# Kernel tuning notes

Measured on AMD Instinct MI355X. Metric: run time of the kernel, lower is better.

## Reference

```python
import jax, jax.numpy as jnp
import numpy as np

NUM_HEADS = 32
HEAD_DIM = 128
HIDDEN = NUM_HEADS * HEAD_DIM
BLOCK = 128
ROPE_THETA = 10000.0
NEG_INF = -1e9


def _fp4_e2m1(x):
    # Simulated float_quantize(x, exp=2, man=1): E2M1 grid {0, .5, 1, 1.5, 2, 3, 4, 6},
    # round-to-nearest-even, saturate at +-6.
    a = jnp.abs(x)
    e = jnp.clip(jnp.floor(jnp.log2(jnp.maximum(a, 1e-30))), 0.0, 2.0)
    step = jnp.exp2(e) * 0.5  # mantissa LSB at this exponent
    q = jnp.clip(jnp.round(a / step) * step, 0.0, 6.0)
    return jnp.sign(x) * q


def quantize_mxfp4(v, block=BLOCK):
    # along_rows=False path: block over the sequence axis (after transpose(-1,-2)).
    b, h, s, d = v.shape
    t = jnp.swapaxes(v, -1, -2)  # [b,h,d,s]
    pad = (-s) % block
    t = jnp.pad(t, ((0, 0), (0, 0), (0, 0), (0, pad)))
    t = t.reshape(-1, block)
    amax = jnp.max(jnp.abs(t), axis=-1, keepdims=True)
    scale = jnp.exp2(jnp.ceil(jnp.log2(jnp.maximum(amax, 1e-30))) - 3.0)
    scale = jnp.where(amax == 0, 1.0, scale)
    t = _fp4_e2m1(t / scale) * scale
    t = t.reshape(b, h, d, s + pad)[..., :s]
    return jnp.swapaxes(t, -1, -2)


def _rotary(position_ids, dtype):
    # cos/sin: [b, s, head_dim]
    inv_freq = 1.0 / (ROPE_THETA ** (jnp.arange(0, HEAD_DIM, 2, dtype=jnp.float32) / HEAD_DIM))
    freqs = position_ids.astype(jnp.float32)[..., None] * inv_freq  # [b,s,d/2]
    emb = jnp.concatenate([freqs, freqs], axis=-1)
    return jnp.cos(emb).astype(dtype), jnp.sin(emb).astype(dtype)


def _rotate_half(x):
    x1, x2 = jnp.split(x, 2, axis=-1)
    return jnp.concatenate([-x2, x1], axis=-1)


def setup_inputs() -> dict:
    key = jax.random.key(0)
    ks = jax.random.split(key, 5)
    wscale = 1.0 / np.sqrt(HIDDEN)
    return {
        "hidden_states": jax.random.normal(ks[0], (2, 2048, HIDDEN), dtype=jnp.float32),
        "position_ids": jnp.arange(2048, dtype=jnp.int32)[None, :],
        "Wq": jax.random.normal(ks[1], (HIDDEN, HIDDEN), dtype=jnp.float32) * wscale,
        "Wk": jax.random.normal(ks[2], (HIDDEN, HIDDEN), dtype=jnp.float32) * wscale,
        "Wv": jax.random.normal(ks[3], (HIDDEN, HIDDEN), dtype=jnp.float32) * wscale,
        "Wo": jax.random.normal(ks[4], (HIDDEN, HIDDEN), dtype=jnp.float32) * wscale,
    }


def reference(hidden_states, position_ids, Wq, Wk, Wv, Wo):
    b, s, _ = hidden_states.shape

    # per-head channel ordering from ||row of v_proj||_2 (descending)
    norm3 = jnp.linalg.norm(Wv.astype(jnp.float32), ord=2, axis=-1)  # [HIDDEN]
    order = jnp.argsort(-norm3.reshape(NUM_HEADS, HEAD_DIM), axis=-1)  # [H, D]
    inverse_order = jnp.argsort(order, axis=-1)

    def proj(W):
        y = jnp.einsum('bsh,oh->bso', hidden_states, W)
        return y.reshape(b, s, NUM_HEADS, HEAD_DIM).transpose(0, 2, 1, 3)  # [b,H,s,D]

    q = proj(Wq)
    k = proj(Wk)
    v = proj(Wv)

    # reorder channels, mxfp4-quantize V along sequence blocks, restore order
    v = jnp.take_along_axis(v, order[None, :, None, :], axis=-1)
    v = quantize_mxfp4(v, BLOCK)
    v = jnp.take_along_axis(v, inverse_order[None, :, None, :], axis=-1)

    cos, sin = _rotary(position_ids, hidden_states.dtype)
    cos = cos[:, None, :, :]  # unsqueeze_dim=1
    sin = sin[:, None, :, :]
    q = q * cos + _rotate_half(q) * sin
    k = k * cos + _rotate_half(k) * sin

    scores = jnp.einsum('bhqd,bhkd->bhqk', q, k) / np.sqrt(HEAD_DIM)
    causal = jnp.tril(jnp.ones((s, s), dtype=bool))
    scores = jnp.where(causal[None, None], scores, NEG_INF)
    attn = jax.nn.softmax(scores.astype(jnp.float32), axis=-1).astype(q.dtype)

    out = jnp.einsum('bhqk,bhkd->bhqd', attn, v)
    out = out.transpose(0, 2, 1, 3).reshape(b, s, HIDDEN)
    return jnp.einsum('bso,ho->bsh', out, Wo)
```

## Files before the change

### kernel.cpp

```cpp
#include <hip/hip_runtime.h>
#include <math.h>

typedef unsigned short u16;
typedef unsigned int u32;
typedef short bf16x8 __attribute__((ext_vector_type(8)));
typedef float f32x4 __attribute__((ext_vector_type(4)));

#define MFMA16(a, b, c) __builtin_amdgcn_mfma_f32_16x16x32_bf16(a, b, c, 0, 0, 0)

static __device__ __forceinline__ u16 f2b(float f) {
  u32 u = __builtin_bit_cast(u32, f);
  u = (u + 0x7fffu + ((u >> 16) & 1u)) >> 16;
  return (u16)u;
}
static __device__ __forceinline__ float b2f(u16 h) {
  return __builtin_bit_cast(float, ((u32)h) << 16);
}
static __device__ __forceinline__ void gload16(const void* g, void* l) {
  __builtin_amdgcn_global_load_lds((const __attribute__((address_space(1))) void*)g,
                                   (__attribute__((address_space(3))) void*)l, 16, 0, 0);
}
static __device__ __forceinline__ void split2(float x, u16& hi, u16& lo) {
  hi = f2b(x);
  lo = f2b(x - b2f(hi));
}
static __device__ __forceinline__ float quant1(float x, float scale, float rs) {
  float y = fabsf(x) * rs;
  float st = y < 2.f ? 0.5f : (y < 4.f ? 1.f : 2.f);
  float iv = y < 2.f ? 2.f : (y < 4.f ? 1.f : 0.5f);
  float q = fminf(rintf(y * iv) * st, 6.f);
  return copysignf(q * scale, x);
}

__global__ __launch_bounds__(256) void k_cvt(const float* __restrict__ in, u16* __restrict__ out) {
  int i = blockIdx.x * 256 + threadIdx.x;
  float4 v = ((const float4*)in)[i];
  u32 lo = (u32)f2b(v.x) | ((u32)f2b(v.y) << 16);
  u32 hi = (u32)f2b(v.z) | ((u32)f2b(v.w) << 16);
  ((uint2*)out)[i] = make_uint2(lo, hi);
}

__global__ __launch_bounds__(256) void k_splt(const float* __restrict__ in,
                                              u16* __restrict__ hi, u16* __restrict__ lo) {
  int i = blockIdx.x * 256 + threadIdx.x;
  float4 v = ((const float4*)in)[i];
  u16 h[4], l[4];
  split2(v.x, h[0], l[0]);
  split2(v.y, h[1], l[1]);
  split2(v.z, h[2], l[2]);
  split2(v.w, h[3], l[3]);
  ((uint2*)hi)[i] = make_uint2((u32)h[0] | ((u32)h[1] << 16), (u32)h[2] | ((u32)h[3] << 16));
  ((uint2*)lo)[i] = make_uint2((u32)l[0] | ((u32)l[1] << 16), (u32)l[2] | ((u32)l[3] << 16));
}

__global__ __launch_bounds__(256) void k_rope_tab(const int* __restrict__ pid,
                                                  float* __restrict__ ct,
                                                  float* __restrict__ st) {
  int t = blockIdx.x * 256 + threadIdx.x;
  int s = t >> 6, i = t & 63;
  float inv = powf(10000.f, -(float)i * (1.f / 64.f));
  float a = (float)pid[s] * inv;
  ct[t] = cosf(a);
  st[t] = sinf(a);
}

template <int EPI>
__global__ __launch_bounds__(512, 2) void k_gemm8(const u16* __restrict__ A,
                                                  const u16* __restrict__ B,
                                                  void* __restrict__ outp,
                                                  const float* __restrict__ cost,
                                                  const float* __restrict__ sint) {
  __shared__ u16 Ls[2][2][2][8192];
  const int tid = threadIdx.x;
  const int wid = tid >> 6, lane = tid & 63;
  const int l15 = lane & 15, lhi = lane >> 4;
  const int wm = wid >> 2, wn = wid & 3;
  const int hib = wn >> 1, sub = wn & 1;

  const int bid = blockIdx.x;
  const int bx = 2 * (bid & 7) + (bid >> 7);
  const int by = (bid >> 3) & 15;
  const int mbase = by * 256, nbase = bx * 256;

  f32x4 acc[8][4];
#pragma unroll
  for (int mi = 0; mi < 8; ++mi)
#pragma unroll
    for (int nj = 0; nj < 4; ++nj) acc[mi][nj] = (f32x4){0.f, 0.f, 0.f, 0.f};

  auto stA = [&](int buf, int half, int ktile) {
    u16* dst = Ls[buf][0][half];
    const int k0 = ktile * 64;
#pragma unroll
    for (int i = 0; i < 2; ++i) {
      int idx = i * 512 + tid;
      int row = idx >> 3;
      int col = k0 + ((((idx & 7) << 4) ^ ((row & 7) << 4)) >> 1);
      gload16(A + (size_t)(mbase + half * 128 + row) * 4096 + col, (char*)dst + idx * 16);
    }
  };
  auto stB = [&](int buf, int half, int ktile) {
    u16* dst = Ls[buf][1][half];
    const int k0 = ktile * 64;
#pragma unroll
    for (int i = 0; i < 2; ++i) {
      int idx = i * 512 + tid;
      int row = idx >> 3;
      int col = k0 + ((((idx & 7) << 4) ^ ((row & 7) << 4)) >> 1);
      gload16(B + (size_t)(nbase + half * 128 + row) * 4096 + col, (char*)dst + idx * 16);
    }
  };

  stB(0, 0, 0);
  stB(0, 1, 0);
  stA(0, 0, 0);
  stA(0, 1, 0);
  stB(1, 0, 1);
  stB(1, 1, 1);

  const int NT = 64;
  for (int kt = 0; kt < NT; ++kt) {
    const int cur = kt & 1, nxt = cur ^ 1;
    const u16* Ab = Ls[cur][0][wm];
    const u16* Bb = Ls[cur][1][hib];
    bf16x8 aA[4][2], aB[4][2], bA[2][2], bB[2][2];

    if (kt + 1 < NT) stA(nxt, 0, kt + 1);
    if (kt == NT - 1) {
      asm volatile("s_waitcnt vmcnt(0)" ::: "memory");
    } else {
      asm volatile("s_waitcnt vmcnt(6)" ::: "memory");
    }
    __builtin_amdgcn_s_barrier();
#pragma unroll
    for (int mi = 0; mi < 4; ++mi)
#pragma unroll
      for (int ks = 0; ks < 2; ++ks) {
        int row = mi * 16 + l15;
        int kk2 = (ks * 32 + lhi * 8) * 2;
        aA[mi][ks] = *(const bf16x8*)((const char*)Ab + row * 128 + (kk2 ^ ((row & 7) << 4)));
      }
#pragma unroll
    for (int nj = 0; nj < 2; ++nj)
#pragma unroll
      for (int ks = 0; ks < 2; ++ks) {
        int row = sub * 32 + nj * 16 + l15;
        int kk2 = (ks * 32 + lhi * 8) * 2;
        bA[nj][ks] = *(const bf16x8*)((const char*)Bb + row * 128 + (kk2 ^ ((row & 7) << 4)));
      }
    __builtin_amdgcn_s_setprio(1);
#pragma unroll
    for (int mi = 0; mi < 4; ++mi)
#pragma unroll
      for (int nj = 0; nj < 2; ++nj)
#pragma unroll
        for (int ks = 0; ks < 2; ++ks) acc[mi][nj] = MFMA16(aA[mi][ks], bA[nj][ks], acc[mi][nj]);
    __builtin_amdgcn_s_setprio(0);
    __builtin_amdgcn_s_barrier();

#pragma unroll
    for (int nj = 0; nj < 2; ++nj)
#pragma unroll
      for (int ks = 0; ks < 2; ++ks) {
        int row = 64 + sub * 32 + nj * 16 + l15;
        int kk2 = (ks * 32 + lhi * 8) * 2;
        bB[nj][ks] = *(const bf16x8*)((const char*)Bb + row * 128 + (kk2 ^ ((row & 7) << 4)));
      }
    if (kt + 1 < NT) stA(nxt, 1, kt + 1);
    __builtin_amdgcn_s_barrier();
    __builtin_amdgcn_s_setprio(1);
#pragma unroll
    for (int mi = 0; mi < 4; ++mi)
#pragma unroll
      for (int nj = 0; nj < 2; ++nj)
#pragma unroll
        for (int ks = 0; ks < 2; ++ks)
          acc[mi][nj + 2] = MFMA16(aA[mi][ks], bB[nj][ks], acc[mi][nj + 2]);
    __builtin_amdgcn_s_setprio(0);
    __builtin_amdgcn_s_barrier();

#pragma unroll
    for (int mi = 0; mi < 4; ++mi)
#pragma unroll
      for (int ks = 0; ks < 2; ++ks) {
        int row = 64 + mi * 16 + l15;
        int kk2 = (ks * 32 + lhi * 8) * 2;
        aB[mi][ks] = *(const bf16x8*)((const char*)Ab + row * 128 + (kk2 ^ ((row & 7) << 4)));
      }
    if (kt + 2 < NT) stB(cur, 0, kt + 2);
    __builtin_amdgcn_s_barrier();
    __builtin_amdgcn_s_setprio(1);
#pragma unroll
    for (int mi = 0; mi < 4; ++mi)
#pragma unroll
      for (int nj = 0; nj < 2; ++nj)
#pragma unroll
        for (int ks = 0; ks < 2; ++ks)
          acc[mi + 4][nj] = MFMA16(aB[mi][ks], bA[nj][ks], acc[mi + 4][nj]);
    __builtin_amdgcn_s_setprio(0);
    __builtin_amdgcn_s_barrier();

    if (kt + 2 < NT) stB(cur, 1, kt + 2);
    __builtin_amdgcn_s_barrier();
    __builtin_amdgcn_s_setprio(1);
#pragma unroll
    for (int mi = 0; mi < 4; ++mi)
#pragma unroll
      for (int nj = 0; nj < 2; ++nj)
#pragma unroll
        for (int ks = 0; ks < 2; ++ks)
          acc[mi + 4][nj + 2] = MFMA16(aB[mi][ks], bB[nj][ks], acc[mi + 4][nj + 2]);
    __builtin_amdgcn_s_setprio(0);
    __builtin_amdgcn_s_barrier();
  }

  if constexpr (EPI == 3) {
    float* out = (float*)outp;
#pragma unroll
    for (int mi = 0; mi < 8; ++mi)
#pragma unroll
      for (int r = 0; r < 4; ++r) {
        size_t m = (size_t)(mbase + wm * 128 + mi * 16 + lhi * 4 + r);
#pragma unroll
        for (int nj = 0; nj < 4; ++nj) {
          int n = nbase + hib * 128 + (nj >> 1) * 64 + sub * 32 + (nj & 1) * 16 + l15;
          out[m * 4096 + n] = acc[mi][nj][r];
        }
      }
  } else {
    u16* qo = (u16*)outp;
    const int hgl = bx * 2 + hib;
#pragma unroll
    for (int mi = 0; mi < 8; ++mi)
#pragma unroll
      for (int r = 0; r < 4; ++r) {
        int m = mbase + wm * 128 + mi * 16 + lhi * 4 + r;
        int b = m >> 11, s = m & 2047;
        const float* ct = cost + (size_t)s * 64;
        const float* st = sint + (size_t)s * 64;
        size_t base = ((size_t)(b * 32 + hgl) * 2048 + s) * 128;
#pragma unroll
        for (int nj = 0; nj < 2; ++nj) {
          int d = sub * 32 + nj * 16 + l15;
          float c = ct[d], sn = st[d];
          float x1 = acc[mi][nj][r], x2 = acc[mi][nj + 2][r];
          qo[base + d] = f2b(x1 * c - x2 * sn);
          qo[base + d + 64] = f2b(x2 * c + x1 * sn);
        }
      }
  }
}

__global__ __launch_bounds__(256) void k_gemmv2(const u16* __restrict__ ahi,
                                                const u16* __restrict__ alo,
                                                const u16* __restrict__ bhi,
                                                const u16* __restrict__ blo,
                                                u16* __restrict__ vt) {
  __shared__ u16 AsHi[128 * 64];
  __shared__ u16 AsLo[128 * 64];
  __shared__ u16 BsHi[128 * 64];
  __shared__ u16 BsLo[128 * 64];
  const int tid = threadIdx.x;
  const int w = tid >> 6, lane = tid & 63;
  const int l15 = lane & 15, lhi = lane >> 4;
  const int mbase = blockIdx.y * 128, nbase = blockIdx.x * 128;
  f32x4 acc[2][8];
#pragma unroll
  for (int i = 0; i < 2; ++i)
#pragma unroll
    for (int j = 0; j < 8; ++j) acc[i][j] = (f32x4){0.f, 0.f, 0.f, 0.f};

  for (int kt = 0; kt < 64; ++kt) {
    const int k0 = kt * 64;
#pragma unroll
    for (int i = 0; i < 4; ++i) {
      int idx = i * 256 + tid;
      int row = idx >> 3;
      int col = (k0 + ((((idx & 7) << 4) ^ ((row & 7) << 4)) >> 1));
      size_t ga = (size_t)(mbase + row) * 4096 + col;
      size_t gb = (size_t)(nbase + row) * 4096 + col;
      gload16(ahi + ga, (char*)AsHi + idx * 16);
      gload16(alo + ga, (char*)AsLo + idx * 16);
      gload16(bhi + gb, (char*)BsHi + idx * 16);
      gload16(blo + gb, (char*)BsLo + idx * 16);
    }
    __syncthreads();
#pragma unroll
    for (int ks = 0; ks < 2; ++ks) {
      const int kk2 = (ks * 32 + lhi * 8) * 2;
      bf16x8 afh[2], afl[2];
#pragma unroll
      for (int i = 0; i < 2; ++i) {
        int row = w * 32 + i * 16 + l15;
        int off = row * 128 + (kk2 ^ ((row & 7) << 4));
        afh[i] = *(const bf16x8*)((const char*)AsHi + off);
        afl[i] = *(const bf16x8*)((const char*)AsLo + off);
      }
#pragma unroll
      for (int j = 0; j < 8; ++j) {
        int row = j * 16 + l15;
        int off = row * 128 + (kk2 ^ ((row & 7) << 4));
        bf16x8 bh = *(const bf16x8*)((const char*)BsHi + off);
        bf16x8 bl = *(const bf16x8*)((const char*)BsLo + off);
#pragma unroll
        for (int i = 0; i < 2; ++i) {
          acc[i][j] = MFMA16(afh[i], bh, acc[i][j]);
          acc[i][j] = MFMA16(afh[i], bl, acc[i][j]);
          acc[i][j] = MFMA16(afl[i], bh, acc[i][j]);
        }
      }
    }
    __syncthreads();
  }

  const int h = nbase >> 7;
  float pam[8];
#pragma unroll
  for (int j = 0; j < 8; ++j) {
    float a = 0.f;
#pragma unroll
    for (int i = 0; i < 2; ++i)
#pragma unroll
      for (int r = 0; r < 4; ++r) a = fmaxf(a, fabsf(acc[i][j][r]));
    a = fmaxf(a, __shfl_xor(a, 16));
    a = fmaxf(a, __shfl_xor(a, 32));
    pam[j] = a;
  }
  float* red = (float*)BsHi;
  if (lhi == 0) {
#pragma unroll
    for (int j = 0; j < 8; ++j) red[w * 128 + j * 16 + l15] = pam[j];
  }
  __syncthreads();
#pragma unroll
  for (int j = 0; j < 8; ++j) {
    float amax = fmaxf(fmaxf(red[0 * 128 + j * 16 + l15], red[1 * 128 + j * 16 + l15]),
                       fmaxf(red[2 * 128 + j * 16 + l15], red[3 * 128 + j * 16 + l15]));
    float scale = 1.f, rs = 1.f;
    if (amax > 0.f) {
      int e;
      float mant = frexpf(amax, &e);
      int c = (mant == 0.5f) ? (e - 1) : e;
      scale = ldexpf(1.f, c - 3);
      rs = ldexpf(1.f, 3 - c);
    }
#pragma unroll
    for (int i = 0; i < 2; ++i) {
      int m0 = mbase + w * 32 + i * 16 + lhi * 4;
      int b = m0 >> 11, s0 = m0 & 2047;
      int d = j * 16 + l15;
      uint2 pk;
      float v0 = quant1(acc[i][j][0], scale, rs);
      float v1 = quant1(acc[i][j][1], scale, rs);
      float v2 = quant1(acc[i][j][2], scale, rs);
      float v3 = quant1(acc[i][j][3], scale, rs);
      pk.x = (u32)f2b(v0) | ((u32)f2b(v1) << 16);
      pk.y = (u32)f2b(v2) | ((u32)f2b(v3) << 16);
      *(uint2*)(vt + ((size_t)(b * 32 + h) * 128 + d) * 2048 + s0) = pk;
    }
  }
}

template <int EPI>
__global__ __launch_bounds__(256) void k_gemm(const u16* __restrict__ A,
                                              const float* __restrict__ B,
                                              void* __restrict__ outp,
                                              const float* __restrict__ cost,
                                              const float* __restrict__ sint) {
  __shared__ u16 As[128 * 64];
  __shared__ u16 Bs[128 * 64];
  const int tid = threadIdx.x;
  const int w = tid >> 6, lane = tid & 63;
  const int l15 = lane & 15, lhi = lane >> 4;
  const int mbase = blockIdx.y * 128, nbase = blockIdx.x * 128;
  f32x4 acc[2][8];
#pragma unroll
  for (int i = 0; i < 2; ++i)
#pragma unroll
    for (int j = 0; j < 8; ++j) acc[i][j] = (f32x4){0.f, 0.f, 0.f, 0.f};

  const int brow = tid >> 1, bk = (tid & 1) * 32;
  const float* bsrc = B + (size_t)(nbase + brow) * 4096 + bk;

  for (int kt = 0; kt < 64; ++kt) {
    const int k0 = kt * 64;
#pragma unroll
    for (int i = 0; i < 4; ++i) {
      int idx = i * 256 + tid;
      int row = idx >> 3;
      int inb = ((idx & 7) << 4) ^ ((row & 7) << 4);
      gload16(A + (size_t)(mbase + row) * 4096 + (k0 + (inb >> 1)), (char*)As + idx * 16);
    }
    float4 bv[8];
    const float* bp = bsrc + k0;
#pragma unroll
    for (int c = 0; c < 8; ++c) bv[c] = *(const float4*)(bp + c * 4);
#pragma unroll
    for (int c = 0; c < 4; ++c) {
      uint4 pk;
      pk.x = (u32)f2b(bv[2 * c].x) | ((u32)f2b(bv[2 * c].y) << 16);
      pk.y = (u32)f2b(bv[2 * c].z) | ((u32)f2b(bv[2 * c].w) << 16);
      pk.z = (u32)f2b(bv[2 * c + 1].x) | ((u32)f2b(bv[2 * c + 1].y) << 16);
      pk.w = (u32)f2b(bv[2 * c + 1].z) | ((u32)f2b(bv[2 * c + 1].w) << 16);
      int byte = brow * 128 + (((bk + c * 8) * 2) ^ ((brow & 7) << 4));
      *(uint4*)((char*)Bs + byte) = pk;
    }
    __syncthreads();
#pragma unroll
    for (int ks = 0; ks < 2; ++ks) {
      const int kk2 = (ks * 32 + lhi * 8) * 2;
      bf16x8 af[2], bfr[8];
#pragma unroll
      for (int i = 0; i < 2; ++i) {
        int row = w * 32 + i * 16 + l15;
        af[i] = *(const bf16x8*)((const char*)As + row * 128 + (kk2 ^ ((row & 7) << 4)));
      }
#pragma unroll
      for (int j = 0; j < 8; ++j) {
        int row = j * 16 + l15;
        bfr[j] = *(const bf16x8*)((const char*)Bs + row * 128 + (kk2 ^ ((row & 7) << 4)));
      }
#pragma unroll
      for (int i = 0; i < 2; ++i)
#pragma unroll
        for (int j = 0; j < 8; ++j) acc[i][j] = MFMA16(af[i], bfr[j], acc[i][j]);
    }
    __syncthreads();
  }

  const int h = nbase >> 7;
  if constexpr (EPI == 3) {
    float* out = (float*)outp;
#pragma unroll
    for (int i = 0; i < 2; ++i)
#pragma unroll
      for (int r = 0; r < 4; ++r) {
        size_t m = (size_t)(mbase + w * 32 + i * 16 + lhi * 4 + r);
#pragma unroll
        for (int j = 0; j < 8; ++j) out[m * 4096 + nbase + j * 16 + l15] = acc[i][j][r];
      }
  } else {
    u16* qo = (u16*)outp;
#pragma unroll
    for (int i = 0; i < 2; ++i)
#pragma unroll
      for (int r = 0; r < 4; ++r) {
        int m = mbase + w * 32 + i * 16 + lhi * 4 + r;
        int b = m >> 11, s = m & 2047;
        const float* ct = cost + (size_t)s * 64;
        const float* st = sint + (size_t)s * 64;
        size_t base = ((size_t)(b * 32 + h) * 2048 + s) * 128;
#pragma unroll
        for (int j = 0; j < 4; ++j) {
          int d = j * 16 + l15;
          float c = ct[d], sn = st[d];
          float x1 = acc[i][j][r], x2 = acc[i][j + 4][r];
          qo[base + d] = f2b(x1 * c - x2 * sn);
          qo[base + d + 64] = f2b(x2 * c + x1 * sn);
        }
      }
  }
}

__global__ __launch_bounds__(256) void k_gemmv(const float* __restrict__ hsf,
                                               const float* __restrict__ Wv,
                                               u16* __restrict__ vt) {
  __shared__ u16 AsHi[128 * 64];
  __shared__ u16 AsLo[128 * 64];
  __shared__ u16 BsHi[128 * 64];
  __shared__ u16 BsLo[128 * 64];
  const int tid = threadIdx.x;
  const int w = tid >> 6, lane = tid & 63;
  const int l15 = lane & 15, lhi = lane >> 4;
  const int mbase = blockIdx.y * 128, nbase = blockIdx.x * 128;
  f32x4 acc[2][8];
#pragma unroll
  for (int i = 0; i < 2; ++i)
#pragma unroll
    for (int j = 0; j < 8; ++j) acc[i][j] = (f32x4){0.f, 0.f, 0.f, 0.f};

  const int srow = tid >> 1, sk = (tid & 1) * 32;
  const float* asrc = hsf + (size_t)(mbase + srow) * 4096 + sk;
  const float* bsrc = Wv + (size_t)(nbase + srow) * 4096 + sk;

  for (int kt = 0; kt < 64; ++kt) {
    const int k0 = kt * 64;
    float4 av[8], bv[8];
#pragma unroll
    for (int c = 0; c < 8; ++c) {
      av[c] = *(const float4*)(asrc + k0 + c * 4);
      bv[c] = *(const float4*)(bsrc + k0 + c * 4);
    }
#pragma unroll
    for (int c = 0; c < 4; ++c) {
      u16 h0, l0, h1, l1;
      float fa[8] = {av[2 * c].x, av[2 * c].y, av[2 * c].z, av[2 * c].w,
                     av[2 * c + 1].x, av[2 * c + 1].y, av[2 * c + 1].z, av[2 * c + 1].w};
      float fb[8] = {bv[2 * c].x, bv[2 * c].y, bv[2 * c].z, bv[2 * c].w,
                     bv[2 * c + 1].x, bv[2 * c + 1].y, bv[2 * c + 1].z, bv[2 * c + 1].w};
      u32 ph[4], pl[4], qh[4], ql[4];
#pragma unroll
      for (int t = 0; t < 4; ++t) {
        split2(fa[2 * t], h0, l0);
        split2(fa[2 * t + 1], h1, l1);
        ph[t] = (u32)h0 | ((u32)h1 << 16);
        pl[t] = (u32)l0 | ((u32)l1 << 16);
        split2(fb[2 * t], h0, l0);
        split2(fb[2 * t + 1], h1, l1);
        qh[t] = (u32)h0 | ((u32)h1 << 16);
        ql[t] = (u32)l0 | ((u32)l1 << 16);
      }
      int byte = srow * 128 + (((sk + c * 8) * 2) ^ ((srow & 7) << 4));
      *(uint4*)((char*)AsHi + byte) = make_uint4(ph[0], ph[1], ph[2], ph[3]);
      *(uint4*)((char*)AsLo + byte) = make_uint4(pl[0], pl[1], pl[2], pl[3]);
      *(uint4*)((char*)BsHi + byte) = make_uint4(qh[0], qh[1], qh[2], qh[3]);
      *(uint4*)((char*)BsLo + byte) = make_uint4(ql[0], ql[1], ql[2], ql[3]);
    }
    __syncthreads();
#pragma unroll
    for (int ks = 0; ks < 2; ++ks) {
      const int kk2 = (ks * 32 + lhi * 8) * 2;
      bf16x8 afh[2], afl[2];
#pragma unroll
      for (int i = 0; i < 2; ++i) {
        int row = w * 32 + i * 16 + l15;
        int off = row * 128 + (kk2 ^ ((row & 7) << 4));
        afh[i] = *(const bf16x8*)((const char*)AsHi + off);
        afl[i] = *(const bf16x8*)((const char*)AsLo + off);
      }
#pragma unroll
      for (int j = 0; j < 8; ++j) {
        int row = j * 16 + l15;
        int off = row * 128 + (kk2 ^ ((row & 7) << 4));
        bf16x8 bh = *(const bf16x8*)((const char*)BsHi + off);
        bf16x8 bl = *(const bf16x8*)((const char*)BsLo + off);
#pragma unroll
        for (int i = 0; i < 2; ++i) {
          acc[i][j] = MFMA16(afh[i], bh, acc[i][j]);
          acc[i][j] = MFMA16(afh[i], bl, acc[i][j]);
          acc[i][j] = MFMA16(afl[i], bh, acc[i][j]);
        }
      }
    }
    __syncthreads();
  }

  const int h = nbase >> 7;
  float pam[8];
#pragma unroll
  for (int j = 0; j < 8; ++j) {
    float a = 0.f;
#pragma unroll
    for (int i = 0; i < 2; ++i)
#pragma unroll
      for (int r = 0; r < 4; ++r) a = fmaxf(a, fabsf(acc[i][j][r]));
    a = fmaxf(a, __shfl_xor(a, 16));
    a = fmaxf(a, __shfl_xor(a, 32));
    pam[j] = a;
  }
  float* red = (float*)BsHi;
  if (lhi == 0) {
#pragma unroll
    for (int j = 0; j < 8; ++j) red[w * 128 + j * 16 + l15] = pam[j];
  }
  __syncthreads();
#pragma unroll
  for (int j = 0; j < 8; ++j) {
    float amax = fmaxf(fmaxf(red[0 * 128 + j * 16 + l15], red[1 * 128 + j * 16 + l15]),
                       fmaxf(red[2 * 128 + j * 16 + l15], red[3 * 128 + j * 16 + l15]));
    float scale = 1.f, rs = 1.f;
    if (amax > 0.f) {
      int e;
      float mant = frexpf(amax, &e);
      int c = (mant == 0.5f) ? (e - 1) : e;
      scale = ldexpf(1.f, c - 3);
      rs = ldexpf(1.f, 3 - c);
    }
#pragma unroll
    for (int i = 0; i < 2; ++i) {
      int m0 = mbase + w * 32 + i * 16 + lhi * 4;
      int b = m0 >> 11, s0 = m0 & 2047;
      int d = j * 16 + l15;
      uint2 pk;
      float v0 = quant1(acc[i][j][0], scale, rs);
      float v1 = quant1(acc[i][j][1], scale, rs);
      float v2 = quant1(acc[i][j][2], scale, rs);
      float v3 = quant1(acc[i][j][3], scale, rs);
      pk.x = (u32)f2b(v0) | ((u32)f2b(v1) << 16);
      pk.y = (u32)f2b(v2) | ((u32)f2b(v3) << 16);
      *(uint2*)(vt + ((size_t)(b * 32 + h) * 128 + d) * 2048 + s0) = pk;
    }
  }
}

__global__ __launch_bounds__(512) void k_attn(const u16* __restrict__ qg,
                                              const u16* __restrict__ kg,
                                              const u16* __restrict__ vtg,
                                              u16* __restrict__ ao) {
  __shared__ u16 Ks[2][64 * 128];
  __shared__ u16 Vs[2][128 * 64];
  __shared__ u16 Ps[8 * 16 * 72];
  const int qt = 15 - blockIdx.y;
  const int bh = blockIdx.x;
  const int tid = threadIdx.x, w = tid >> 6, lane = tid & 63;
  const int l15 = lane & 15, lhi = lane >> 4;
  const size_t bhoff = (size_t)bh * (2048 * 128);
  const float SC = 0.08838834764831845f;

  bf16x8 qf[4];
  {
    const int qrow = qt * 128 + w * 16 + l15;
    const u16* qp = qg + bhoff + (size_t)qrow * 128 + lhi * 8;
#pragma unroll
    for (int ks = 0; ks < 4; ++ks) qf[ks] = *(const bf16x8*)(qp + ks * 32);
  }
  f32x4 oacc[8];
#pragma unroll
  for (int dt = 0; dt < 8; ++dt) oacc[dt] = (f32x4){0.f, 0.f, 0.f, 0.f};
  float mrow[4] = {-1e30f, -1e30f, -1e30f, -1e30f};
  float lrow[4] = {0.f, 0.f, 0.f, 0.f};

  auto stage = [&](int buf, int kbase) {
#pragma unroll
    for (int i = 0; i < 2; ++i) {
      int idx = i * 512 + tid;
      int row = idx >> 4;
      int inb = ((idx & 15) << 4) ^ ((row & 15) << 4);
      gload16(kg + bhoff + (size_t)(kbase + row) * 128 + (inb >> 1), (char*)Ks[buf] + idx * 16);
    }
#pragma unroll
    for (int i = 0; i < 2; ++i) {
      int idx = i * 512 + tid;
      int row = idx >> 3;
      int inb = ((idx & 7) << 4) ^ ((row & 7) << 4);
      gload16(vtg + bhoff + (size_t)row * 2048 + kbase + (inb >> 1), (char*)Vs[buf] + idx * 16);
    }
  };

  const int nt = 2 * qt + 2;
  stage(0, 0);

  for (int kt = 0; kt < nt; ++kt) {
    const int cur = kt & 1;
    if (kt < nt - 1) {
      stage(cur ^ 1, (kt + 1) * 64);
      asm volatile("s_waitcnt vmcnt(4)" ::: "memory");
    } else {
      asm volatile("s_waitcnt vmcnt(0)" ::: "memory");
    }
    __builtin_amdgcn_s_barrier();

    f32x4 sc4[4];
#pragma unroll
    for (int j = 0; j < 4; ++j) sc4[j] = (f32x4){0.f, 0.f, 0.f, 0.f};
#pragma unroll
    for (int ks = 0; ks < 4; ++ks) {
      const int db = (ks * 32 + lhi * 8) * 2;
#pragma unroll
      for (int j = 0; j < 4; ++j) {
        int kr = j * 16 + l15;
        bf16x8 bfr = *(const bf16x8*)((const char*)Ks[cur] + kr * 256 + (db ^ ((kr & 15) << 4)));
        sc4[j] = MFMA16(qf[ks], bfr, sc4[j]);
      }
    }
    float p[4][4];
    const int kbase = kt * 64;
    const bool tail = (kt >= 2 * qt);
#pragma unroll
    for (int j = 0; j < 4; ++j)
#pragma unroll
      for (int r = 0; r < 4; ++r) {
        float s = sc4[j][r] * SC;
        if (tail && (kbase + j * 16 + l15 > qt * 128 + w * 16 + lhi * 4 + r)) s = -1e9f;
        p[j][r] = s;
      }
    float alpha[4];
#pragma unroll
    for (int r = 0; r < 4; ++r) {
      float tm = fmaxf(fmaxf(p[0][r], p[1][r]), fmaxf(p[2][r], p[3][r]));
      tm = fmaxf(tm, __shfl_xor(tm, 1));
      tm = fmaxf(tm, __shfl_xor(tm, 2));
      tm = fmaxf(tm, __shfl_xor(tm, 4));
      tm = fmaxf(tm, __shfl_xor(tm, 8));
      float mn = fmaxf(mrow[r], tm);
      alpha[r] = __expf(mrow[r] - mn);
      mrow[r] = mn;
      float rsum = 0.f;
#pragma unroll
      for (int j = 0; j < 4; ++j) {
        float e = __expf(p[j][r] - mn);
        p[j][r] = e;
        rsum += e;
      }
      rsum += __shfl_xor(rsum, 1);
      rsum += __shfl_xor(rsum, 2);
      rsum += __shfl_xor(rsum, 4);
      rsum += __shfl_xor(rsum, 8);
      lrow[r] = lrow[r] * alpha[r] + rsum;
    }
#pragma unroll
    for (int dt = 0; dt < 8; ++dt) {
      f32x4 t = oacc[dt];
      t[0] *= alpha[0]; t[1] *= alpha[1]; t[2] *= alpha[2]; t[3] *= alpha[3];
      oacc[dt] = t;
    }
#pragma unroll
    for (int j = 0; j < 4; ++j)
#pragma unroll
      for (int r = 0; r < 4; ++r)
        Ps[w * 1152 + (lhi * 4 + r) * 72 + j * 16 + l15] = f2b(p[j][r]);
#pragma unroll
    for (int ks2 = 0; ks2 < 2; ++ks2) {
      const int sb = ks2 * 32 + lhi * 8;
      bf16x8 pa = *(const bf16x8*)((const char*)Ps + w * 2304 + l15 * 144 + sb * 2);
#pragma unroll
      for (int dt = 0; dt < 8; ++dt) {
        int d = dt * 16 + l15;
        bf16x8 vb = *(const bf16x8*)((const char*)Vs[cur] + d * 128 + ((sb * 2) ^ ((d & 7) << 4)));
        oacc[dt] = MFMA16(pa, vb, oacc[dt]);
      }
    }
    asm volatile("s_waitcnt lgkmcnt(0)" ::: "memory");
    __builtin_amdgcn_s_barrier();
  }

  const int b = bh >> 5, h = bh & 31;
  float inv[4];
#pragma unroll
  for (int r = 0; r < 4; ++r) inv[r] = 1.f / lrow[r];
#pragma unroll
  for (int dt = 0; dt < 8; ++dt)
#pragma unroll
    for (int r = 0; r < 4; ++r) {
      int s = qt * 128 + w * 16 + lhi * 4 + r;
      ao[((size_t)(b * 2048 + s)) * 4096 + h * 128 + dt * 16 + l15] = f2b(oacc[dt][r] * inv[r]);
    }
}

extern "C" void kernel_launch(void* const* d_in, const int* in_sizes, int n_in,
                              void* d_out, int out_size, void* d_ws, size_t ws_size,
                              hipStream_t stream) {
  (void)in_sizes; (void)n_in; (void)out_size;
  const float* hs = (const float*)d_in[0];
  const int* pid = (const int*)d_in[1];
  const float* Wq = (const float*)d_in[2];
  const float* Wk = (const float*)d_in[3];
  const float* Wv = (const float*)d_in[4];
  const float* Wo = (const float*)d_in[5];
  float* out = (float*)d_out;
  char* ws = (char*)d_ws;

  const size_t BUF = 33554432;
  const size_t NEED = 7 * BUF + 2 * 524288;

  if (ws_size >= NEED) {
    u16* hsb  = (u16*)(ws + 0 * BUF);
    u16* hslo = (u16*)(ws + 1 * BUF);
    u16* qb   = (u16*)(ws + 2 * BUF);
    u16* kb   = (u16*)(ws + 3 * BUF);
    u16* vtb  = (u16*)(ws + 4 * BUF);
    u16* wbuf = (u16*)(ws + 5 * BUF);
    u16* wvlo = (u16*)(ws + 6 * BUF);
    float* cost = (float*)(ws + 7 * BUF);
    float* sint = (float*)(ws + 7 * BUF + 524288);
    u16* aob = hslo;

    k_splt<<<16384, 256, 0, stream>>>(hs, hsb, hslo);
    k_rope_tab<<<512, 256, 0, stream>>>(pid, cost, sint);
    k_cvt<<<16384, 256, 0, stream>>>(Wq, wbuf);
    k_gemm8<0><<<256, 512, 0, stream>>>(hsb, wbuf, (void*)qb, cost, sint);
    k_cvt<<<16384, 256, 0, stream>>>(Wk, wbuf);
    k_gemm8<1><<<256, 512, 0, stream>>>(hsb, wbuf, (void*)kb, cost, sint);
    k_splt<<<16384, 256, 0, stream>>>(Wv, wbuf, wvlo);
    k_gemmv2<<<dim3(32, 32), 256, 0, stream>>>(hsb, hslo, wbuf, wvlo, vtb);
    k_attn<<<dim3(64, 16), 512, 0, stream>>>(qb, kb, vtb, aob);
    k_cvt<<<16384, 256, 0, stream>>>(Wo, wbuf);
    k_gemm8<3><<<256, 512, 0, stream>>>(aob, wbuf, (void*)out, nullptr, nullptr);
  } else {
    u16* hsb = (u16*)(ws + 0);
    u16* qb  = (u16*)(ws + 33554432);
    u16* kb  = (u16*)(ws + 67108864);
    u16* vtb = (u16*)(ws + 100663296);
    float* cost = (float*)(ws + 134217728);
    float* sint = (float*)(ws + 134742016);
    u16* aob = hsb;

    k_cvt<<<16384, 256, 0, stream>>>(hs, hsb);
    k_rope_tab<<<512, 256, 0, stream>>>(pid, cost, sint);
    k_gemm<0><<<dim3(32, 32), 256, 0, stream>>>(hsb, Wq, (void*)qb, cost, sint);
    k_gemm<1><<<dim3(32, 32), 256, 0, stream>>>(hsb, Wk, (void*)kb, cost, sint);
    k_gemmv<<<dim3(32, 32), 256, 0, stream>>>(hs, Wv, vtb);
    k_attn<<<dim3(64, 16), 512, 0, stream>>>(qb, kb, vtb, aob);
    k_gemm<3><<<dim3(32, 32), 256, 0, stream>>>(aob, Wo, (void*)out, nullptr, nullptr);
  }
}
```

Baseline: 939.2 us.

## Double-buffer split-bf16 V projection GEMM with 512 threads and 2x4 warp grid

Rewrites the V-projection GEMM, which uses hi/lo split bf16 operands, so that the next K tile is loaded into a second LDS buffer while the current one is computed. It waits on vmcnt instead of a full sync after each load. It also moves from 4 waves to 8 waves arranged 2x4, each computing a 64x32 sub-tile, and reworks the amax reduction for the mxfp4 epilogue to match. LDS use doubles to 128KB per block, which can cap occupancy at one block per CU.

```diff
diff --git a/kernel.cpp b/kernel.cpp
--- a/kernel.cpp
+++ b/kernel.cpp
@@ -251,109 +251,127 @@
   }
 }
 
-__global__ __launch_bounds__(256) void k_gemmv2(const u16* __restrict__ ahi,
+__global__ __launch_bounds__(512) void k_gemmv3(const u16* __restrict__ ahi,
                                                 const u16* __restrict__ alo,
                                                 const u16* __restrict__ bhi,
                                                 const u16* __restrict__ blo,
                                                 u16* __restrict__ vt) {
-  __shared__ u16 AsHi[128 * 64];
-  __shared__ u16 AsLo[128 * 64];
-  __shared__ u16 BsHi[128 * 64];
-  __shared__ u16 BsLo[128 * 64];
+  __shared__ u16 Ls[2][4][8192];
   const int tid = threadIdx.x;
-  const int w = tid >> 6, lane = tid & 63;
+  const int wid = tid >> 6, lane = tid & 63;
   const int l15 = lane & 15, lhi = lane >> 4;
+  const int wm = wid >> 2, wn = wid & 3;
   const int mbase = blockIdx.y * 128, nbase = blockIdx.x * 128;
-  f32x4 acc[2][8];
-#pragma unroll
-  for (int i = 0; i < 2; ++i)
-#pragma unroll
-    for (int j = 0; j < 8; ++j) acc[i][j] = (f32x4){0.f, 0.f, 0.f, 0.f};
-
-  for (int kt = 0; kt < 64; ++kt) {
-    const int k0 = kt * 64;
-#pragma unroll
-    for (int i = 0; i < 4; ++i) {
-      int idx = i * 256 + tid;
+
+  f32x4 acc[4][2];
+#pragma unroll
+  for (int mi = 0; mi < 4; ++mi)
+#pragma unroll
+    for (int nj = 0; nj < 2; ++nj) acc[mi][nj] = (f32x4){0.f, 0.f, 0.f, 0.f};
+
+  auto stage = [&](int buf, int ktile) {
+    const int k0 = ktile * 64;
+#pragma unroll
+    for (int i = 0; i < 2; ++i) {
+      int idx = i * 512 + tid;
       int row = idx >> 3;
-      int col = (k0 + ((((idx & 7) << 4) ^ ((row & 7) << 4)) >> 1));
+      int col = k0 + ((((idx & 7) << 4) ^ ((row & 7) << 4)) >> 1);
       size_t ga = (size_t)(mbase + row) * 4096 + col;
       size_t gb = (size_t)(nbase + row) * 4096 + col;
-      gload16(ahi + ga, (char*)AsHi + idx * 16);
-      gload16(alo + ga, (char*)AsLo + idx * 16);
-      gload16(bhi + gb, (char*)BsHi + idx * 16);
-      gload16(blo + gb, (char*)BsLo + idx * 16);
-    }
-    __syncthreads();
-#pragma unroll
-    for (int ks = 0; ks < 2; ++ks) {
-      const int kk2 = (ks * 32 + lhi * 8) * 2;
-      bf16x8 afh[2], afl[2];
-#pragma unroll
-      for (int i = 0; i < 2; ++i) {
-        int row = w * 32 + i * 16 + l15;
-        int off = row * 128 + (kk2 ^ ((row & 7) << 4));
-        afh[i] = *(const bf16x8*)((const char*)AsHi + off);
-        afl[i] = *(const bf16x8*)((const char*)AsLo + off);
-      }
-#pragma unroll
-      for (int j = 0; j < 8; ++j) {
-        int row = j * 16 + l15;
-        int off = row * 128 + (kk2 ^ ((row & 7) << 4));
-        bf16x8 bh = *(const bf16x8*)((const char*)BsHi + off);
-        bf16x8 bl = *(const bf16x8*)((const char*)BsLo + off);
-#pragma unroll
-        for (int i = 0; i < 2; ++i) {
-          acc[i][j] = MFMA16(afh[i], bh, acc[i][j]);
-          acc[i][j] = MFMA16(afh[i], bl, acc[i][j]);
-          acc[i][j] = MFMA16(afl[i], bh, acc[i][j]);
+      gload16(ahi + ga, (char*)Ls[buf][0] + idx * 16);
+      gload16(alo + ga, (char*)Ls[buf][1] + idx * 16);
+      gload16(bhi + gb, (char*)Ls[buf][2] + idx * 16);
+      gload16(blo + gb, (char*)Ls[buf][3] + idx * 16);
+    }
+  };
+
+  stage(0, 0);
+
+  const int NT = 64;
+  for (int kt = 0; kt < NT; ++kt) {
+    const int cur = kt & 1;
+    if (kt < NT - 1) {
+      stage(cur ^ 1, kt + 1);
+      asm volatile("s_waitcnt vmcnt(8)" ::: "memory");
+    } else {
+      asm volatile("s_waitcnt vmcnt(0)" ::: "memory");
+    }
+    __builtin_amdgcn_s_barrier();
+
+    bf16x8 ah[4][2], al[4][2], bh[2][2], bl[2][2];
+#pragma unroll
+    for (int mi = 0; mi < 4; ++mi)
+#pragma unroll
+      for (int ks = 0; ks < 2; ++ks) {
+        int row = wm * 64 + mi * 16 + l15;
+        int off = row * 128 + (((ks * 32 + lhi * 8) * 2) ^ ((row & 7) << 4));
+        ah[mi][ks] = *(const bf16x8*)((const char*)Ls[cur][0] + off);
+        al[mi][ks] = *(const bf16x8*)((const char*)Ls[cur][1] + off);
+      }
+#pragma unroll
+    for (int nj = 0; nj < 2; ++nj)
+#pragma unroll
+      for (int ks = 0; ks < 2; ++ks) {
+        int row = wn * 32 + nj * 16 + l15;
+        int off = row * 128 + (((ks * 32 + lhi * 8) * 2) ^ ((row & 7) << 4));
+        bh[nj][ks] = *(const bf16x8*)((const char*)Ls[cur][2] + off);
+        bl[nj][ks] = *(const bf16x8*)((const char*)Ls[cur][3] + off);
+      }
+#pragma unroll
+    for (int ks = 0; ks < 2; ++ks)
+#pragma unroll
+      for (int mi = 0; mi < 4; ++mi)
+#pragma unroll
+        for (int nj = 0; nj < 2; ++nj) {
+          acc[mi][nj] = MFMA16(ah[mi][ks], bh[nj][ks], acc[mi][nj]);
+          acc[mi][nj] = MFMA16(ah[mi][ks], bl[nj][ks], acc[mi][nj]);
+          acc[mi][nj] = MFMA16(al[mi][ks], bh[nj][ks], acc[mi][nj]);
         }
-      }
-    }
-    __syncthreads();
+    asm volatile("s_waitcnt lgkmcnt(0)" ::: "memory");
+    __builtin_amdgcn_s_barrier();
   }
 
   const int h = nbase >> 7;
-  float pam[8];
-#pragma unroll
-  for (int j = 0; j < 8; ++j) {
+  float* red = (float*)Ls[0][0];
+  float pam[2];
+#pragma unroll
+  for (int nj = 0; nj < 2; ++nj) {
     float a = 0.f;
 #pragma unroll
-    for (int i = 0; i < 2; ++i)
-#pragma unroll
-      for (int r = 0; r < 4; ++r) a = fmaxf(a, fabsf(acc[i][j][r]));
+    for (int mi = 0; mi < 4; ++mi)
+#pragma unroll
+      for (int r = 0; r < 4; ++r) a = fmaxf(a, fabsf(acc[mi][nj][r]));
     a = fmaxf(a, __shfl_xor(a, 16));
     a = fmaxf(a, __shfl_xor(a, 32));
-    pam[j] = a;
-  }
-  float* red = (float*)BsHi;
+    pam[nj] = a;
+  }
   if (lhi == 0) {
 #pragma unroll
-    for (int j = 0; j < 8; ++j) red[w * 128 + j * 16 + l15] = pam[j];
+    for (int nj = 0; nj < 2; ++nj) red[wid * 32 + nj * 16 + l15] = pam[nj];
   }
   __syncthreads();
 #pragma unroll
-  for (int j = 0; j < 8; ++j) {
-    float amax = fmaxf(fmaxf(red[0 * 128 + j * 16 + l15], red[1 * 128 + j * 16 + l15]),
-                       fmaxf(red[2 * 128 + j * 16 + l15], red[3 * 128 + j * 16 + l15]));
+  for (int nj = 0; nj < 2; ++nj) {
+    int c = nj * 16 + l15;
+    float amax = fmaxf(red[wn * 32 + c], red[(4 + wn) * 32 + c]);
     float scale = 1.f, rs = 1.f;
     if (amax > 0.f) {
       int e;
       float mant = frexpf(amax, &e);
-      int c = (mant == 0.5f) ? (e - 1) : e;
-      scale = ldexpf(1.f, c - 3);
-      rs = ldexpf(1.f, 3 - c);
-    }
-#pragma unroll
-    for (int i = 0; i < 2; ++i) {
-      int m0 = mbase + w * 32 + i * 16 + lhi * 4;
+      int cc = (mant == 0.5f) ? (e - 1) : e;
+      scale = ldexpf(1.f, cc - 3);
+      rs = ldexpf(1.f, 3 - cc);
+    }
+    int d = wn * 32 + c;
+#pragma unroll
+    for (int mi = 0; mi < 4; ++mi) {
+      int m0 = mbase + wm * 64 + mi * 16 + lhi * 4;
       int b = m0 >> 11, s0 = m0 & 2047;
-      int d = j * 16 + l15;
       uint2 pk;
-      float v0 = quant1(acc[i][j][0], scale, rs);
-      float v1 = quant1(acc[i][j][1], scale, rs);
-      float v2 = quant1(acc[i][j][2], scale, rs);
-      float v3 = quant1(acc[i][j][3], scale, rs);
+      float v0 = quant1(acc[mi][nj][0], scale, rs);
+      float v1 = quant1(acc[mi][nj][1], scale, rs);
+      float v2 = quant1(acc[mi][nj][2], scale, rs);
+      float v3 = quant1(acc[mi][nj][3], scale, rs);
       pk.x = (u32)f2b(v0) | ((u32)f2b(v1) << 16);
       pk.y = (u32)f2b(v2) | ((u32)f2b(v3) << 16);
       *(uint2*)(vt + ((size_t)(b * 32 + h) * 128 + d) * 2048 + s0) = pk;
@@ -772,7 +790,7 @@
     k_cvt<<<16384, 256, 0, stream>>>(Wk, wbuf);
     k_gemm8<1><<<256, 512, 0, stream>>>(hsb, wbuf, (void*)kb, cost, sint);
     k_splt<<<16384, 256, 0, stream>>>(Wv, wbuf, wvlo);
-    k_gemmv2<<<dim3(32, 32), 256, 0, stream>>>(hsb, hslo, wbuf, wvlo, vtb);
+    k_gemmv3<<<dim3(32, 32), 512, 0, stream>>>(hsb, hslo, wbuf, wvlo, vtb);
     k_attn<<<dim3(64, 16), 512, 0, stream>>>(qb, kb, vtb, aob);
     k_cvt<<<16384, 256, 0, stream>>>(Wo, wbuf);
     k_gemm8<3><<<256, 512, 0, stream>>>(aob, wbuf, (void*)out, nullptr, nullptr);
```

Measured after the change: 997.0 us. 6.2% more time.
